# Optimization experiments

Measured on AMD Instinct MI355X. Metric: run time of the kernel, lower is better.

## Reference

```python
import jax, jax.numpy as jnp
import numpy as np

D_MODEL = 512
D_STATE = 128
D_CONV = 4
EXPAND = 2
HEADDIM = 64
NGROUPS = 1
D_INNER = EXPAND * D_MODEL            # 1024
NHEADS = D_INNER // HEADDIM           # 16
CONV_DIM = D_INNER + 2 * NGROUPS * D_STATE   # 1280
D_IN_PROJ = 2 * D_INNER + 2 * NGROUPS * D_STATE + NHEADS  # 2320
EPS = 1e-5


def _silu(v):
    return v * jax.nn.sigmoid(v)


def setup_inputs() -> dict:
    key = jax.random.key(0)
    ks = jax.random.split(key, 8)
    B, L = 2, 1024
    x = jax.random.normal(ks[0], (B, L, D_MODEL), jnp.float32)
    in_proj_w = jax.random.normal(ks[1], (D_IN_PROJ, D_MODEL), jnp.float32) * (D_MODEL ** -0.5)
    conv_w = jax.random.normal(ks[2], (CONV_DIM, D_CONV), jnp.float32) * (D_CONV ** -0.5)
    conv_b = jnp.zeros((CONV_DIM,), jnp.float32)
    # dt_bias = softplus^-1(dt) for dt ~ U[1e-3, 0.1]  (Mamba2 init)
    dt = jax.random.uniform(ks[3], (NHEADS,), jnp.float32, 0.001, 0.1)
    dt_bias = jnp.log(jnp.expm1(dt))
    A_log = jnp.log(jax.random.uniform(ks[4], (NHEADS,), jnp.float32, 1.0, 16.0))
    D = jnp.ones((NHEADS,), jnp.float32)
    norm_w = jnp.ones((D_INNER,), jnp.float32)
    out_proj_w = jax.random.normal(ks[5], (D_MODEL, D_INNER), jnp.float32) * (D_INNER ** -0.5)
    return dict(x=x, in_proj_w=in_proj_w, conv_w=conv_w, conv_b=conv_b,
                dt_bias=dt_bias, A_log=A_log, D=D, norm_w=norm_w, out_proj_w=out_proj_w)


def _mamba2(x, in_proj_w, conv_w, conv_b, dt_bias, A_log, D, norm_w, out_proj_w):
    Bb, L, _ = x.shape
    # input projection -> [z | xBC | dt]
    zxbcdt = jnp.einsum('bld,ed->ble', x, in_proj_w)          # (B,L,2320)
    z = zxbcdt[..., :D_INNER]                                  # (B,L,1024)
    xBC = zxbcdt[..., D_INNER:D_INNER + CONV_DIM]              # (B,L,1280)
    dt = jax.nn.softplus(zxbcdt[..., D_INNER + CONV_DIM:] + dt_bias)  # (B,L,H)
    # causal depthwise conv1d over L + SiLU
    lhs = jnp.transpose(xBC, (0, 2, 1))                        # (B,C,L)
    rhs = conv_w[:, None, :]                                   # (C,1,K)
    conv = jax.lax.conv_general_dilated(
        lhs, rhs, window_strides=(1,), padding=[(D_CONV - 1, 0)],
        dimension_numbers=('NCH', 'OIH', 'NCH'), feature_group_count=CONV_DIM)
    xBC = _silu(jnp.transpose(conv, (0, 2, 1)) + conv_b)       # (B,L,1280)
    xs = xBC[..., :D_INNER].reshape(Bb, L, NHEADS, HEADDIM)    # (B,L,H,P)
    Bmat = xBC[..., D_INNER:D_INNER + D_STATE]                 # (B,L,N) ngroups=1
    Cmat = xBC[..., D_INNER + D_STATE:]                        # (B,L,N)
    # selective scan: h_t = exp(dt_t*A)*h_{t-1} + (dt_t*x_t) outer B_t ; y_t = C_t . h_t
    A = -jnp.exp(A_log)                                        # (H,)
    dA = jnp.exp(dt * A)                                       # (B,L,H)
    dx = dt[..., None] * xs                                    # (B,L,H,P)

    def step(h, inp):
        dA_t, dx_t, B_t, C_t = inp                             # (B,H),(B,H,P),(B,N),(B,N)
        h = h * dA_t[..., None, None] + dx_t[..., None] * B_t[:, None, None, :]
        y = jnp.einsum('bhpn,bn->bhp', h, C_t)
        return h, y

    h0 = jnp.zeros((Bb, NHEADS, HEADDIM, D_STATE), x.dtype)
    _, ys = jax.lax.scan(step, h0, (jnp.moveaxis(dA, 1, 0), jnp.moveaxis(dx, 1, 0),
                                    jnp.moveaxis(Bmat, 1, 0), jnp.moveaxis(Cmat, 1, 0)))
    y = jnp.moveaxis(ys, 0, 1) + xs * D[None, None, :, None]   # (B,L,H,P)
    y = y.reshape(Bb, L, D_INNER)
    # gated RMSNorm: rmsnorm(y * silu(z)) * w
    g = y * _silu(z)
    g = g * jax.lax.rsqrt(jnp.mean(g * g, axis=-1, keepdims=True) + EPS) * norm_w
    return jnp.einsum('ble,de->bld', g, out_proj_w)            # (B,L,d_model)


def reference(x, in_proj_w, conv_w, conv_b, dt_bias, A_log, D, norm_w, out_proj_w):
    return _mamba2(x, in_proj_w, conv_w, conv_b, dt_bias, A_log, D, norm_w, out_proj_w)
```

## Files before the change

kernel.cpp:

```cpp
#include <hip/hip_runtime.h>
#include <math.h>

#define BATCH 2
#define SEQ 1024
#define DM 512
#define DI 1024
#define DS 128
#define NH 16
#define HD 64
#define CONVD 1280
#define DPROJ 2320
#define ROWS (BATCH*SEQ)
#define NCH 16
#define CHK 64
#define NPAD 2432

typedef unsigned short u16;
typedef unsigned int   u32;
typedef u16   u16x4 __attribute__((ext_vector_type(4)));
typedef u16   u16x8 __attribute__((ext_vector_type(8)));
typedef short bf16x8 __attribute__((ext_vector_type(8)));
typedef float f32x4 __attribute__((ext_vector_type(4)));

__device__ __forceinline__ u16 f2bf(float f) {
    u32 u = __float_as_uint(f);
    return (u16)((u + 0x7fffu + ((u >> 16) & 1u)) >> 16);
}
__device__ __forceinline__ float bf2f(u16 h) {
    return __uint_as_float(((u32)h) << 16);
}
__device__ __forceinline__ void gl_lds16(const u16* g, u16* lds) {
    __builtin_amdgcn_global_load_lds((const __attribute__((address_space(1))) void*)g,
                                     (__attribute__((address_space(3))) void*)lds,
                                     16, 0, 0);
}

__device__ __forceinline__ int xcd_swz(int bid, int nwg) {
    int q = nwg >> 3;
    return (bid & 7) * q + (bid >> 3);
}

__device__ __forceinline__ int swz_off(int row, int q, int SLROW) {
    return (row*SLROW + (q ^ (row & 7)))*8;
}
template<int SLROW>
__device__ __forceinline__ void stage64(const u16* gbase, int gstride, u16* lds, int tid) {
    #pragma unroll
    for (int j = 0; j < (64*SLROW)/256; ++j) {
        int slot = j*256 + tid;
        int row = slot / SLROW;
        int pos = slot % SLROW;
        gl_lds16(gbase + (size_t)row*gstride + (pos ^ (row & 7))*8, lds + slot*8);
    }
}

__device__ __forceinline__ void cvt_blk(const float* __restrict__ src,
                                        u16* __restrict__ dst,
                                        int blk, int n_src, int n_total) {
    int idx = (blk*256 + threadIdx.x)*8;
    if (idx >= n_total) return;
    u16x8 o;
    if (idx + 8 <= n_src) {
        float4 a = *reinterpret_cast<const float4*>(src + idx);
        float4 b = *reinterpret_cast<const float4*>(src + idx + 4);
        o[0]=f2bf(a.x); o[1]=f2bf(a.y); o[2]=f2bf(a.z); o[3]=f2bf(a.w);
        o[4]=f2bf(b.x); o[5]=f2bf(b.y); o[6]=f2bf(b.z); o[7]=f2bf(b.w);
    } else {
        #pragma unroll
        for (int e = 0; e < 8; ++e)
            o[e] = (idx + e < n_src) ? f2bf(src[idx + e]) : (u16)0;
    }
    *reinterpret_cast<u16x8*>(dst + idx) = o;
}

__global__ __launch_bounds__(256) void k_prep(const float* __restrict__ x,
                                              const float* __restrict__ W,
                                              const float* __restrict__ Wo,
                                              const float* __restrict__ dt_bias,
                                              const float* __restrict__ A_log,
                                              u16* __restrict__ xb,
                                              u16* __restrict__ Wb,
                                              u16* __restrict__ Wob,
                                              float* __restrict__ dtb,
                                              float* __restrict__ abuf) {
    int bid = blockIdx.x;
    if (bid < 512) { cvt_blk(x, xb, bid, ROWS*DM, ROWS*DM); return; }
    if (bid < 1120) { cvt_blk(W, Wb, bid-512, DPROJ*DM, NPAD*DM); return; }
    if (bid < 1376) { cvt_blk(Wo, Wob, bid-1120, DM*DI, DM*DI); return; }
    int wave = threadIdx.x >> 6, lane = threadIdx.x & 63;
    int row = (bid-1376)*4 + wave;
    int h = lane & 15, part = lane >> 4;
    const float* xr = x + (size_t)row * DM + part*128;
    const float* wr = W + (size_t)(DI + CONVD + h) * DM + part*128;
    float acc = 0.f;
    #pragma unroll 4
    for (int j = 0; j < 32; ++j) {
        float4 xv = *reinterpret_cast<const float4*>(xr + j*4);
        float4 wv = *reinterpret_cast<const float4*>(wr + j*4);
        acc += xv.x*wv.x + xv.y*wv.y + xv.z*wv.z + xv.w*wv.w;
    }
    acc += __shfl_xor(acc, 16);
    acc += __shfl_xor(acc, 32);
    if (part == 0) {
        float v = acc + dt_bias[h];
        float dt = (v > 20.f) ? v : log1pf(expf(v));
        dtb[row*NH + h]  = dt;
        abuf[row*NH + h] = dt * (-expf(A_log[h]));
    }
}

template<int BM, int BN, int K, int NBX, bool BF16OUT>
__global__ __launch_bounds__(256) void k_gemm(const u16* __restrict__ A,
                                              const u16* __restrict__ B,
                                              void* __restrict__ Cv,
                                              int ldc, int ncols) {
    constexpr int BK = 64;
    constexpr int NK = K / BK;
    constexpr int WTM = BM/2, WTN = BN/2, FM = WTM/16, FN = WTN/16;
    constexpr int CA = BM/32, CB = BN/32;
    constexpr int TA = BM*8, TB = BN*8;
    __shared__ u16 As[2*TA*8];
    __shared__ u16 Bs[2*TB*8];
    int tid = threadIdx.x, lane = tid & 63, wave = tid >> 6;
    int wr = wave >> 1, wc = wave & 1;

    int nb = xcd_swz(blockIdx.x, gridDim.x);
    size_t bm = (size_t)(nb / NBX) * BM, bn = (size_t)(nb % NBX) * BN;

    const u16* sA[CA]; int dA[CA];
    #pragma unroll
    for (int j = 0; j < CA; ++j) {
        int i = j*256 + tid, row = i >> 3, pos = i & 7;
        sA[j] = A + (bm + row)*(size_t)K + (pos ^ (row & 7))*8;
        dA[j] = i*8;
    }
    const u16* sB[CB]; int dB[CB];
    #pragma unroll
    for (int j = 0; j < CB; ++j) {
        int i = j*256 + tid, row = i >> 3, pos = i & 7;
        sB[j] = B + (bn + row)*(size_t)K + (pos ^ (row & 7))*8;
        dB[j] = i*8;
    }

    int fr = lane & 15, kq = lane >> 4;
    int ar[FM], br[FN];
    #pragma unroll
    for (int fi = 0; fi < FM; ++fi) ar[fi] = wr*WTM + fi*16 + fr;
    #pragma unroll
    for (int fj = 0; fj < FN; ++fj) br[fj] = wc*WTN + fj*16 + fr;

    f32x4 acc[FM][FN];
    #pragma unroll
    for (int fi = 0; fi < FM; ++fi)
        #pragma unroll
        for (int fj = 0; fj < FN; ++fj)
            acc[fi][fj] = (f32x4){0.f,0.f,0.f,0.f};

    #pragma unroll
    for (int j = 0; j < CA; ++j) gl_lds16(sA[j], As + dA[j]);
    #pragma unroll
    for (int j = 0; j < CB; ++j) gl_lds16(sB[j], Bs + dB[j]);
    asm volatile("s_waitcnt vmcnt(0)" ::: "memory");
    __builtin_amdgcn_s_barrier();

    int cur = 0;
    #pragma unroll 1
    for (int step = 0; step < NK; ++step) {
        if (step + 1 < NK) {
            int k0 = (step+1)*BK;
            int nbuf = cur ^ 1;
            #pragma unroll
            for (int j = 0; j < CA; ++j) gl_lds16(sA[j] + k0, As + nbuf*TA*8 + dA[j]);
            #pragma unroll
            for (int j = 0; j < CB; ++j) gl_lds16(sB[j] + k0, Bs + nbuf*TB*8 + dB[j]);
        }
        const u16* Ab = As + cur*TA*8;
        const u16* Bb = Bs + cur*TB*8;
        #pragma unroll
        for (int ks = 0; ks < 2; ++ks) {
            bf16x8 av[FM], bv[FN];
            #pragma unroll
            for (int fi = 0; fi < FM; ++fi)
                av[fi] = *reinterpret_cast<const bf16x8*>(Ab + (ar[fi]*8 + ((ks*4+kq) ^ (ar[fi]&7)))*8);
            #pragma unroll
            for (int fj = 0; fj < FN; ++fj)
                bv[fj] = *reinterpret_cast<const bf16x8*>(Bb + (br[fj]*8 + ((ks*4+kq) ^ (br[fj]&7)))*8);
            #pragma unroll
            for (int fi = 0; fi < FM; ++fi)
                #pragma unroll
                for (int fj = 0; fj < FN; ++fj)
                    acc[fi][fj] = __builtin_amdgcn_mfma_f32_16x16x32_bf16(
                        av[fi], bv[fj], acc[fi][fj], 0, 0, 0);
        }
        asm volatile("s_waitcnt vmcnt(0)" ::: "memory");
        __builtin_amdgcn_s_barrier();
        cur ^= 1;
    }

    #pragma unroll
    for (int fi = 0; fi < FM; ++fi) {
        size_t grow0 = bm + wr*WTM + fi*16 + kq*4;
        #pragma unroll
        for (int fj = 0; fj < FN; ++fj) {
            size_t gcol = bn + wc*WTN + fj*16 + fr;
            if ((int)gcol < ncols) {
                #pragma unroll
                for (int r = 0; r < 4; ++r) {
                    if constexpr (BF16OUT)
                        ((u16*)Cv)[(grow0 + r)*ldc + gcol] = f2bf(acc[fi][fj][r]);
                    else
                        ((float*)Cv)[(grow0 + r)*ldc + gcol] = acc[fi][fj][r];
                }
            }
        }
    }
}

__global__ __launch_bounds__(320) void k_conv(const u16* __restrict__ zx,
                                              const float* __restrict__ cw,
                                              const float* __restrict__ cb,
                                              u16* __restrict__ convo) {
    int row = blockIdx.x;
    int l   = row & (SEQ-1);
    int c0  = threadIdx.x * 4;

    const float4* cw4 = reinterpret_cast<const float4*>(cw);
    float4 w0 = cw4[c0+0], w1 = cw4[c0+1], w2 = cw4[c0+2], w3 = cw4[c0+3];
    const float* wa0 = &w0.x; const float* wa1 = &w1.x;
    const float* wa2 = &w2.x; const float* wa3 = &w3.x;

    float4 bv = *reinterpret_cast<const float4*>(cb + c0);
    float acc0 = bv.x, acc1 = bv.y, acc2 = bv.z, acc3 = bv.w;

    #pragma unroll
    for (int k = 0; k < 4; ++k) {
        int lk = l - 3 + k;
        if (lk < 0) continue;
        u16x4 v = *reinterpret_cast<const u16x4*>(zx + (size_t)(row-3+k)*DPROJ + DI + c0);
        acc0 += bf2f(v[0]) * wa0[k];
        acc1 += bf2f(v[1]) * wa1[k];
        acc2 += bf2f(v[2]) * wa2[k];
        acc3 += bf2f(v[3]) * wa3[k];
    }
    u16x4 o;
    o[0] = f2bf(acc0 / (1.f + expf(-acc0)));
    o[1] = f2bf(acc1 / (1.f + expf(-acc1)));
    o[2] = f2bf(acc2 / (1.f + expf(-acc2)));
    o[3] = f2bf(acc3 / (1.f + expf(-acc3)));
    *reinterpret_cast<u16x4*>(convo + (size_t)row*CONVD + c0) = o;
}

__global__ __launch_bounds__(256) void k_chunk_state(
    const u16* __restrict__ convo, const float* __restrict__ dtb,
    const float* __restrict__ abuf, u16* __restrict__ Sb,
    float* __restrict__ Pbuf) {
    int nb = xcd_swz(blockIdx.x, gridDim.x);
    int h  = nb & (NH-1);
    int c  = (nb >> 4) & (NCH-1);
    int b  = nb >> 8;
    int sidx = c + NCH*(h + NH*b);
    int row0 = b*SEQ + c*CHK;
    int tid = threadIdx.x, lane = tid & 63, wave = tid >> 6;
    int wr = wave >> 1, wc = wave & 1;

    __shared__ u16 xsT[64*64];
    __shared__ u16 BT[128*64];
    __shared__ float s_coef[CHK];

    int st = tid >> 2, q = tid & 3;
    const u16* r = convo + (size_t)(row0 + st)*CONVD;
    u16x8 xa = *reinterpret_cast<const u16x8*>(r + h*HD + q*16);
    u16x8 xc = *reinterpret_cast<const u16x8*>(r + h*HD + q*16 + 8);
    u16x8 b0 = *reinterpret_cast<const u16x8*>(r + DI + q*32);
    u16x8 b1 = *reinterpret_cast<const u16x8*>(r + DI + q*32 + 8);
    u16x8 b2 = *reinterpret_cast<const u16x8*>(r + DI + q*32 + 16);
    u16x8 b3 = *reinterpret_cast<const u16x8*>(r + DI + q*32 + 24);

    if (tid < CHK) {
        float v = abuf[(size_t)(row0 + tid)*NH + h];
        #pragma unroll
        for (int off = 1; off < 64; off <<= 1) {
            float o = __shfl_up(v, off);
            if (tid >= off) v += o;
        }
        float vend = __shfl(v, 63);
        float dt = dtb[(size_t)(row0 + tid)*NH + h];
        s_coef[tid] = dt * expf(vend - v);
        if (tid == 63) Pbuf[sidx] = expf(vend);
    }
    __syncthreads();

    float cf = s_coef[st];
    #pragma unroll
    for (int e = 0; e < 16; ++e) {
        int p = q*16 + e;
        u16 xv = (e < 8) ? xa[e] : xc[e-8];
        xsT[(p*8 + ((st>>3) ^ (p&7)))*8 + (st&7)] = f2bf(cf * bf2f(xv));
    }
    #pragma unroll
    for (int e = 0; e < 32; ++e) {
        int n = q*32 + e;
        u16 bvv = (e < 8) ? b0[e] : (e < 16) ? b1[e-8] : (e < 24) ? b2[e-16] : b3[e-24];
        BT[(n*8 + ((st>>3) ^ (n&7)))*8 + (st&7)] = bvv;
    }
    __syncthreads();

    int kq = lane >> 4, fr = lane & 15;
    f32x4 acc[2][4];
    #pragma unroll
    for (int fi = 0; fi < 2; ++fi)
        #pragma unroll
        for (int fj = 0; fj < 4; ++fj)
            acc[fi][fj] = (f32x4){0.f,0.f,0.f,0.f};

    #pragma unroll
    for (int ks = 0; ks < 2; ++ks) {
        bf16x8 av[2], bv[4];
        #pragma unroll
        for (int fi = 0; fi < 2; ++fi)
            av[fi] = *reinterpret_cast<const bf16x8*>(xsT + swz_off(wr*32 + fi*16 + fr, ks*4 + kq, 8));
        #pragma unroll
        for (int fj = 0; fj < 4; ++fj)
            bv[fj] = *reinterpret_cast<const bf16x8*>(BT + swz_off(wc*64 + fj*16 + fr, ks*4 + kq, 8));
        #pragma unroll
        for (int fi = 0; fi < 2; ++fi)
            #pragma unroll
            for (int fj = 0; fj < 4; ++fj)
                acc[fi][fj] = __builtin_amdgcn_mfma_f32_16x16x32_bf16(av[fi], bv[fj], acc[fi][fj], 0,0,0);
    }

    u16* outp = Sb + (size_t)sidx*(HD*DS);
    #pragma unroll
    for (int fi = 0; fi < 2; ++fi)
        #pragma unroll
        for (int rr = 0; rr < 4; ++rr) {
            int p = wr*32 + fi*16 + kq*4 + rr;
            #pragma unroll
            for (int fj = 0; fj < 4; ++fj) {
                int n = wc*64 + fj*16 + fr;
                outp[(size_t)p*DS + n] = f2bf(acc[fi][fj][rr]);
            }
        }
}

__global__ __launch_bounds__(256) void k_state_pass(u16* __restrict__ Sb,
                                                    const float* __restrict__ Pbuf) {
    int bh = blockIdx.x >> 3, seg = blockIdx.x & 7;
    int off = seg*1024 + threadIdx.x*4;
    u16x4 s[NCH];
    #pragma unroll
    for (int cc = 0; cc < NCH; ++cc)
        s[cc] = *reinterpret_cast<const u16x4*>(Sb + ((size_t)(bh*NCH + cc))*(HD*DS) + off);
    float hr[4] = {0.f,0.f,0.f,0.f};
    #pragma unroll
    for (int cc = 0; cc < NCH; ++cc) {
        u16x4 w = { f2bf(hr[0]), f2bf(hr[1]), f2bf(hr[2]), f2bf(hr[3]) };
        *reinterpret_cast<u16x4*>(Sb + ((size_t)(bh*NCH + cc))*(HD*DS) + off) = w;
        float P = Pbuf[bh*NCH + cc];
        #pragma unroll
        for (int j = 0; j < 4; ++j) hr[j] = hr[j]*P + bf2f(s[cc][j]);
    }
}

__global__ __launch_bounds__(256) void k_chunk_out(
    const u16* __restrict__ convo, const float* __restrict__ dtb,
    const float* __restrict__ abuf, const u16* __restrict__ Sb,
    const float* __restrict__ Dp, u16* __restrict__ ybuf) {
    int nb = xcd_swz(blockIdx.x, gridDim.x);
    int h  = nb & (NH-1);
    int c  = (nb >> 4) & (NCH-1);
    int b  = nb >> 8;
    int sidx = c + NCH*(h + NH*b);
    int row0 = b*SEQ + c*CHK;
    int tid = threadIdx.x, lane = tid & 63, wave = tid >> 6;
    int wr = wave >> 1, wc = wave & 1;

    __shared__ u16 Ct[64*128];
    __shared__ u16 Bh[64*128];
    __shared__ u16 Mt[64*64];
    __shared__ u16 dxT[64*64];
    __shared__ float s_cum[CHK];
    __shared__ float s_dt[CHK];

    const u16* cbase = convo + (size_t)row0*CONVD;

    stage64<16>(cbase + DI + DS, CONVD, Ct, tid);
    stage64<16>(cbase + DI,      CONVD, Bh, tid);

    int st = tid >> 2, q = tid & 3;
    u16x8 xr0 = *reinterpret_cast<const u16x8*>(cbase + (size_t)st*CONVD + h*HD + q*16);
    u16x8 xr1 = *reinterpret_cast<const u16x8*>(cbase + (size_t)st*CONVD + h*HD + q*16 + 8);

    if (tid < CHK) {
        float v = abuf[(size_t)(row0 + tid)*NH + h];
        #pragma unroll
        for (int off = 1; off < 64; off <<= 1) {
            float o = __shfl_up(v, off);
            if (tid >= off) v += o;
        }
        s_cum[tid] = v;
        s_dt[tid] = dtb[(size_t)(row0 + tid)*NH + h];
    }
    __syncthreads();

    #pragma unroll
    for (int e = 0; e < 16; ++e) {
        int p = q*16 + e;
        u16 xv = (e < 8) ? xr0[e] : xr1[e-8];
        dxT[(p*8 + ((st>>3) ^ (p&7)))*8 + (st&7)] = xv;
    }

    int kq = lane >> 4, fr = lane & 15;

    f32x4 macc[2][2];
    #pragma unroll
    for (int fi = 0; fi < 2; ++fi)
        #pragma unroll
        for (int fj = 0; fj < 2; ++fj)
            macc[fi][fj] = (f32x4){0.f,0.f,0.f,0.f};
    #pragma unroll
    for (int ks = 0; ks < 4; ++ks) {
        bf16x8 av[2], bv[2];
        #pragma unroll
        for (int fi = 0; fi < 2; ++fi)
            av[fi] = *reinterpret_cast<const bf16x8*>(Ct + swz_off(wr*32 + fi*16 + fr, ks*4 + kq, 16));
        #pragma unroll
        for (int fj = 0; fj < 2; ++fj)
            bv[fj] = *reinterpret_cast<const bf16x8*>(Bh + swz_off(wc*32 + fj*16 + fr, ks*4 + kq, 16));
        #pragma unroll
        for (int fi = 0; fi < 2; ++fi)
            #pragma unroll
            for (int fj = 0; fj < 2; ++fj)
                macc[fi][fj] = __builtin_amdgcn_mfma_f32_16x16x32_bf16(av[fi], bv[fj], macc[fi][fj], 0,0,0);
    }

    #pragma unroll
    for (int fi = 0; fi < 2; ++fi)
        #pragma unroll
        for (int rr = 0; rr < 4; ++rr) {
            int t = wr*32 + fi*16 + kq*4 + rr;
            float cumt = s_cum[t];
            #pragma unroll
            for (int fj = 0; fj < 2; ++fj) {
                int s = wc*32 + fj*16 + fr;
                float val = (s <= t) ? macc[fi][fj][rr] * expf(cumt - s_cum[s]) * s_dt[s] : 0.f;
                Mt[(t*8 + ((s>>3) ^ (t&7)))*8 + (s&7)] = f2bf(val);
            }
        }
    __syncthreads();

    stage64<16>(Sb + (size_t)sidx*(HD*DS), DS, Bh, tid);

    f32x4 accY[2][2];
    #pragma unroll
    for (int fi = 0; fi < 2; ++fi)
        #pragma unroll
        for (int fj = 0; fj < 2; ++fj)
            accY[fi][fj] = (f32x4){0.f,0.f,0.f,0.f};
    #pragma unroll
    for (int ks = 0; ks < 2; ++ks) {
        bf16x8 av[2], bv[2];
        #pragma unroll
        for (int fi = 0; fi < 2; ++fi)
            av[fi] = *reinterpret_cast<const bf16x8*>(Mt + swz_off(wr*32 + fi*16 + fr, ks*4 + kq, 8));
        #pragma unroll
        for (int fj = 0; fj < 2; ++fj)
            bv[fj] = *reinterpret_cast<const bf16x8*>(dxT + swz_off(wc*32 + fj*16 + fr, ks*4 + kq, 8));
        #pragma unroll
        for (int fi = 0; fi < 2; ++fi)
            #pragma unroll
            for (int fj = 0; fj < 2; ++fj)
                accY[fi][fj] = __builtin_amdgcn_mfma_f32_16x16x32_bf16(av[fi], bv[fj], accY[fi][fj], 0,0,0);
    }
    __syncthreads();

    f32x4 accD[2][2];
    #pragma unroll
    for (int fi = 0; fi < 2; ++fi)
        #pragma unroll
        for (int fj = 0; fj < 2; ++fj)
            accD[fi][fj] = (f32x4){0.f,0.f,0.f,0.f};
    #pragma unroll
    for (int ks = 0; ks < 4; ++ks) {
        bf16x8 av[2], bv[2];
        #pragma unroll
        for (int fi = 0; fi < 2; ++fi)
            av[fi] = *reinterpret_cast<const bf16x8*>(Ct + swz_off(wr*32 + fi*16 + fr, ks*4 + kq, 16));
        #pragma unroll
        for (int fj = 0; fj < 2; ++fj)
            bv[fj] = *reinterpret_cast<const bf16x8*>(Bh + swz_off(wc*32 + fj*16 + fr, ks*4 + kq, 16));
        #pragma unroll
        for (int fi = 0; fi < 2; ++fi)
            #pragma unroll
            for (int fj = 0; fj < 2; ++fj)
                accD[fi][fj] = __builtin_amdgcn_mfma_f32_16x16x32_bf16(av[fi], bv[fj], accD[fi][fj], 0,0,0);
    }

    float Dv = Dp[h];
    #pragma unroll
    for (int fi = 0; fi < 2; ++fi)
        #pragma unroll
        for (int rr = 0; rr < 4; ++rr) {
            int t = wr*32 + fi*16 + kq*4 + rr;
            float et = expf(s_cum[t]);
            #pragma unroll
            for (int fj = 0; fj < 2; ++fj) {
                int p = wc*32 + fj*16 + fr;
                float xs = bf2f(cbase[(size_t)t*CONVD + h*HD + p]);
                float y = accY[fi][fj][rr] + et*accD[fi][fj][rr] + Dv*xs;
                ybuf[(size_t)(row0 + t)*DI + h*HD + p] = f2bf(y);
            }
        }
}

__global__ __launch_bounds__(256) void k_gate(const u16* __restrict__ zx,
                                              const u16* __restrict__ ybuf,
                                              const float* __restrict__ nw,
                                              u16* __restrict__ g) {
    int row = blockIdx.x;
    int t = threadIdx.x;
    const u16* zr = zx + (size_t)row*DPROJ;
    const u16* yr = ybuf + (size_t)row*DI;

    u16x4 zv = *reinterpret_cast<const u16x4*>(zr + t*4);
    u16x4 yv = *reinterpret_cast<const u16x4*>(yr + t*4);
    float gv[4];
    float ss = 0.f;
    #pragma unroll
    for (int j = 0; j < 4; ++j) {
        float z = bf2f(zv[j]), y = bf2f(yv[j]);
        float sz = z / (1.f + expf(-z));
        float gg = y * sz;
        gv[j] = gg;
        ss += gg*gg;
    }
    ss += __shfl_xor(ss, 1);
    ss += __shfl_xor(ss, 2);
    ss += __shfl_xor(ss, 4);
    ss += __shfl_xor(ss, 8);
    ss += __shfl_xor(ss, 16);
    ss += __shfl_xor(ss, 32);
    __shared__ float ls[4];
    if ((t & 63) == 0) ls[t >> 6] = ss;
    __syncthreads();
    float tot = ls[0] + ls[1] + ls[2] + ls[3];
    float scale = rsqrtf(tot * (1.f/DI) + 1e-5f);

    float4 nv = *reinterpret_cast<const float4*>(nw + t*4);
    const float* na = &nv.x;
    u16x4 og = { f2bf(gv[0]*scale*na[0]), f2bf(gv[1]*scale*na[1]),
                 f2bf(gv[2]*scale*na[2]), f2bf(gv[3]*scale*na[3]) };
    *reinterpret_cast<u16x4*>(g + (size_t)row*DI + t*4) = og;
}

extern "C" void kernel_launch(void* const* d_in, const int* in_sizes, int n_in,
                              void* d_out, int out_size, void* d_ws, size_t ws_size,
                              hipStream_t stream) {
    const float* x         = (const float*)d_in[0];
    const float* in_proj_w = (const float*)d_in[1];
    const float* conv_w    = (const float*)d_in[2];
    const float* conv_b    = (const float*)d_in[3];
    const float* dt_bias   = (const float*)d_in[4];
    const float* A_log     = (const float*)d_in[5];
    const float* Dp        = (const float*)d_in[6];
    const float* norm_w    = (const float*)d_in[7];
    const float* out_proj_w= (const float*)d_in[8];
    float* out = (float*)d_out;

    char* p = (char*)d_ws;
    u16*   zxb   = (u16*)p;   p += (size_t)ROWS*DPROJ*2;
    u16*   convo = (u16*)p;   p += (size_t)ROWS*CONVD*2;
    float* dtb   = (float*)p; p += (size_t)ROWS*NH*4;
    float* abuf  = (float*)p; p += (size_t)ROWS*NH*4;
    u16*   ybuf  = (u16*)p;   p += (size_t)ROWS*DI*2;
    u16*   xb    = (u16*)p;   p += (size_t)ROWS*DM*2;
    u16*   Wb    = (u16*)p;   p += (size_t)NPAD*DM*2;
    u16*   Wob   = (u16*)p;   p += (size_t)DM*DI*2;
    u16*   Sb    = (u16*)p;   p += (size_t)BATCH*NH*NCH*HD*DS*2;
    float* Pbuf  = (float*)p; p += 512*4;
    u16*   gb    = (u16*)p;   p += (size_t)ROWS*DI*2;

    k_prep<<<1888, 256, 0, stream>>>(x, in_proj_w, out_proj_w, dt_bias, A_log,
                                     xb, Wb, Wob, dtb, abuf);

    k_gemm<64,128,512,19,true><<<(NPAD/128)*(ROWS/64), 256, 0, stream>>>(xb, Wb, zxb, DPROJ, DPROJ);

    k_conv<<<ROWS, CONVD/4, 0, stream>>>(zxb, conv_w, conv_b, convo);

    k_chunk_state<<<BATCH*NH*NCH, 256, 0, stream>>>(convo, dtb, abuf, Sb, Pbuf);
    k_state_pass <<<BATCH*NH*8, 256, 0, stream>>>(Sb, Pbuf);
    k_chunk_out  <<<BATCH*NH*NCH, 256, 0, stream>>>(convo, dtb, abuf, Sb, Dp, ybuf);

    k_gate<<<ROWS, 256, 0, stream>>>(zxb, ybuf, norm_w, gb);

    k_gemm<64,64,1024,8,false><<<(DM/64)*(ROWS/64), 256, 0, stream>>>(gb, Wob, out, DM, DM);
}
```

Baseline: 75.70 us.

## Fuse gated RMSNorm into out-projection GEMM, fold norm weight into Wo

Removes the separate gating/RMSNorm kernel. The out-projection GEMM now builds y*silu(z) on the fly while staging its A tile and accumulates per-row sums of squares during the K loop. The RMS scale is applied to the accumulator in the epilogue, and norm_w is folded into the bf16 weight conversion. This saves one launch and a full round trip of the gated tensor through global memory, but every N-block recomputes the silu gating (8x redundant) and the A staging is now register-based rather than direct-to-LDS.

```diff
diff --git a/kernel.cpp b/kernel.cpp
--- a/kernel.cpp
+++ b/kernel.cpp
@@ -76,6 +76,7 @@
 __global__ __launch_bounds__(256) void k_prep(const float* __restrict__ x,
                                               const float* __restrict__ W,
                                               const float* __restrict__ Wo,
+                                              const float* __restrict__ nw,
                                               const float* __restrict__ dt_bias,
                                               const float* __restrict__ A_log,
                                               u16* __restrict__ xb,
@@ -86,7 +87,19 @@
     int bid = blockIdx.x;
     if (bid < 512) { cvt_blk(x, xb, bid, ROWS*DM, ROWS*DM); return; }
     if (bid < 1120) { cvt_blk(W, Wb, bid-512, DPROJ*DM, NPAD*DM); return; }
-    if (bid < 1376) { cvt_blk(Wo, Wob, bid-1120, DM*DI, DM*DI); return; }
+    if (bid < 1376) {
+        int idx = ((bid-1120)*256 + threadIdx.x)*8;
+        int e = idx & (DI-1);
+        float4 a = *reinterpret_cast<const float4*>(Wo + idx);
+        float4 b = *reinterpret_cast<const float4*>(Wo + idx + 4);
+        float4 na = *reinterpret_cast<const float4*>(nw + e);
+        float4 nb = *reinterpret_cast<const float4*>(nw + e + 4);
+        u16x8 o;
+        o[0]=f2bf(a.x*na.x); o[1]=f2bf(a.y*na.y); o[2]=f2bf(a.z*na.z); o[3]=f2bf(a.w*na.w);
+        o[4]=f2bf(b.x*nb.x); o[5]=f2bf(b.y*nb.y); o[6]=f2bf(b.z*nb.z); o[7]=f2bf(b.w*nb.w);
+        *reinterpret_cast<u16x8*>(Wob + idx) = o;
+        return;
+    }
     int wave = threadIdx.x >> 6, lane = threadIdx.x & 63;
     int row = (bid-1376)*4 + wave;
     int h = lane & 15, part = lane >> 4;
@@ -216,6 +229,140 @@
     }
 }
 
+__global__ __launch_bounds__(256) void k_outproj_gate(
+    const u16* __restrict__ ybuf, const u16* __restrict__ zxb,
+    const u16* __restrict__ Wob, float* __restrict__ out) {
+    constexpr int BM=64, BN=64, K=1024, BK=64, NK=K/BK, NBX=DM/BN;
+    constexpr int FM=2, FN=2;
+    constexpr int TA = BM*8, TB = BN*8;
+    __shared__ u16 As[2*TA*8];
+    __shared__ u16 Bs[2*TB*8];
+    __shared__ float s_ssq[BM];
+    int tid = threadIdx.x, lane = tid & 63, wave = tid >> 6;
+    int wr = wave >> 1, wc = wave & 1;
+
+    int nb = xcd_swz(blockIdx.x, gridDim.x);
+    size_t bm = (size_t)(nb / NBX) * BM, bn = (size_t)(nb % NBX) * BN;
+
+    int r = tid >> 2, qd = tid & 3;
+    const u16* yrow = ybuf + (bm + r)*(size_t)DI + qd*16;
+    const u16* zrow = zxb + (bm + r)*(size_t)DPROJ + qd*16;
+    int aslot0 = (r*8 + ((2*qd)   ^ (r & 7)))*8;
+    int aslot1 = (r*8 + ((2*qd+1) ^ (r & 7)))*8;
+
+    const u16* sB[2]; int dB[2];
+    #pragma unroll
+    for (int j = 0; j < 2; ++j) {
+        int i = j*256 + tid, row = i >> 3, pos = i & 7;
+        sB[j] = Wob + (bn + row)*(size_t)K + (pos ^ (row & 7))*8;
+        dB[j] = i*8;
+    }
+
+    int fr = lane & 15, kq = lane >> 4;
+    int ar[FM], br[FN];
+    #pragma unroll
+    for (int fi = 0; fi < FM; ++fi) ar[fi] = wr*32 + fi*16 + fr;
+    #pragma unroll
+    for (int fj = 0; fj < FN; ++fj) br[fj] = wc*32 + fj*16 + fr;
+
+    f32x4 acc[FM][FN];
+    #pragma unroll
+    for (int fi = 0; fi < FM; ++fi)
+        #pragma unroll
+        for (int fj = 0; fj < FN; ++fj)
+            acc[fi][fj] = (f32x4){0.f,0.f,0.f,0.f};
+
+    float ssq = 0.f;
+    auto STAGE_A = [&](int buf, u16x8 ya, u16x8 yb, u16x8 za, u16x8 zb) {
+        u16x8 o0, o1;
+        #pragma unroll
+        for (int e = 0; e < 8; ++e) {
+            float y = bf2f(ya[e]), z = bf2f(za[e]);
+            float gg = y * (z / (1.f + expf(-z)));
+            ssq += gg*gg;
+            o0[e] = f2bf(gg);
+        }
+        #pragma unroll
+        for (int e = 0; e < 8; ++e) {
+            float y = bf2f(yb[e]), z = bf2f(zb[e]);
+            float gg = y * (z / (1.f + expf(-z)));
+            ssq += gg*gg;
+            o1[e] = f2bf(gg);
+        }
+        u16* dst = As + buf*TA*8;
+        *reinterpret_cast<u16x8*>(dst + aslot0) = o0;
+        *reinterpret_cast<u16x8*>(dst + aslot1) = o1;
+    };
+
+    #pragma unroll
+    for (int j = 0; j < 2; ++j) gl_lds16(sB[j], Bs + dB[j]);
+    {
+        u16x8 ya = *reinterpret_cast<const u16x8*>(yrow);
+        u16x8 yb = *reinterpret_cast<const u16x8*>(yrow + 8);
+        u16x8 za = *reinterpret_cast<const u16x8*>(zrow);
+        u16x8 zb = *reinterpret_cast<const u16x8*>(zrow + 8);
+        STAGE_A(0, ya, yb, za, zb);
+    }
+    __syncthreads();
+
+    int cur = 0;
+    #pragma unroll 1
+    for (int step = 0; step < NK; ++step) {
+        u16x8 nya, nyb, nza, nzb;
+        bool has_next = (step + 1 < NK);
+        if (has_next) {
+            int k0 = (step+1)*BK;
+            #pragma unroll
+            for (int j = 0; j < 2; ++j) gl_lds16(sB[j] + k0, Bs + (cur^1)*TB*8 + dB[j]);
+            nya = *reinterpret_cast<const u16x8*>(yrow + k0);
+            nyb = *reinterpret_cast<const u16x8*>(yrow + k0 + 8);
+            nza = *reinterpret_cast<const u16x8*>(zrow + k0);
+            nzb = *reinterpret_cast<const u16x8*>(zrow + k0 + 8);
+        }
+        const u16* Ab = As + cur*TA*8;
+        const u16* Bb = Bs + cur*TB*8;
+        #pragma unroll
+        for (int ks = 0; ks < 2; ++ks) {
+            bf16x8 av[FM], bv[FN];
+            #pragma unroll
+            for (int fi = 0; fi < FM; ++fi)
+                av[fi] = *reinterpret_cast<const bf16x8*>(Ab + (ar[fi]*8 + ((ks*4+kq) ^ (ar[fi]&7)))*8);
+            #pragma unroll
+            for (int fj = 0; fj < FN; ++fj)
+                bv[fj] = *reinterpret_cast<const bf16x8*>(Bb + (br[fj]*8 + ((ks*4+kq) ^ (br[fj]&7)))*8);
+            #pragma unroll
+            for (int fi = 0; fi < FM; ++fi)
+                #pragma unroll
+                for (int fj = 0; fj < FN; ++fj)
+                    acc[fi][fj] = __builtin_amdgcn_mfma_f32_16x16x32_bf16(
+                        av[fi], bv[fj], acc[fi][fj], 0, 0, 0);
+        }
+        if (has_next) STAGE_A(cur^1, nya, nyb, nza, nzb);
+        __syncthreads();
+        cur ^= 1;
+    }
+
+    ssq += __shfl_xor(ssq, 1);
+    ssq += __shfl_xor(ssq, 2);
+    if (qd == 0) s_ssq[r] = ssq;
+    __syncthreads();
+
+    #pragma unroll
+    for (int fi = 0; fi < FM; ++fi) {
+        #pragma unroll
+        for (int rr = 0; rr < 4; ++rr) {
+            int lr = wr*32 + fi*16 + kq*4 + rr;
+            float scale = rsqrtf(s_ssq[lr]*(1.f/DI) + 1e-5f);
+            size_t grow = bm + lr;
+            #pragma unroll
+            for (int fj = 0; fj < FN; ++fj) {
+                size_t gcol = bn + wc*32 + fj*16 + fr;
+                out[grow*DM + gcol] = scale * acc[fi][fj][rr];
+            }
+        }
+    }
+}
+
 __global__ __launch_bounds__(320) void k_conv(const u16* __restrict__ zx,
                                               const float* __restrict__ cw,
                                               const float* __restrict__ cb,
@@ -511,46 +658,6 @@
                 ybuf[(size_t)(row0 + t)*DI + h*HD + p] = f2bf(y);
             }
         }
-}
-
-__global__ __launch_bounds__(256) void k_gate(const u16* __restrict__ zx,
-                                              const u16* __restrict__ ybuf,
-                                              const float* __restrict__ nw,
-                                              u16* __restrict__ g) {
-    int row = blockIdx.x;
-    int t = threadIdx.x;
-    const u16* zr = zx + (size_t)row*DPROJ;
-    const u16* yr = ybuf + (size_t)row*DI;
-
-    u16x4 zv = *reinterpret_cast<const u16x4*>(zr + t*4);
-    u16x4 yv = *reinterpret_cast<const u16x4*>(yr + t*4);
-    float gv[4];
-    float ss = 0.f;
-    #pragma unroll
-    for (int j = 0; j < 4; ++j) {
-        float z = bf2f(zv[j]), y = bf2f(yv[j]);
-        float sz = z / (1.f + expf(-z));
-        float gg = y * sz;
-        gv[j] = gg;
-        ss += gg*gg;
-    }
-    ss += __shfl_xor(ss, 1);
-    ss += __shfl_xor(ss, 2);
-    ss += __shfl_xor(ss, 4);
-    ss += __shfl_xor(ss, 8);
-    ss += __shfl_xor(ss, 16);
-    ss += __shfl_xor(ss, 32);
-    __shared__ float ls[4];
-    if ((t & 63) == 0) ls[t >> 6] = ss;
-    __syncthreads();
-    float tot = ls[0] + ls[1] + ls[2] + ls[3];
-    float scale = rsqrtf(tot * (1.f/DI) + 1e-5f);
-
-    float4 nv = *reinterpret_cast<const float4*>(nw + t*4);
-    const float* na = &nv.x;
-    u16x4 og = { f2bf(gv[0]*scale*na[0]), f2bf(gv[1]*scale*na[1]),
-                 f2bf(gv[2]*scale*na[2]), f2bf(gv[3]*scale*na[3]) };
-    *reinterpret_cast<u16x4*>(g + (size_t)row*DI + t*4) = og;
 }
 
 extern "C" void kernel_launch(void* const* d_in, const int* in_sizes, int n_in,
@@ -578,9 +685,8 @@
     u16*   Wob   = (u16*)p;   p += (size_t)DM*DI*2;
     u16*   Sb    = (u16*)p;   p += (size_t)BATCH*NH*NCH*HD*DS*2;
     float* Pbuf  = (float*)p; p += 512*4;
-    u16*   gb    = (u16*)p;   p += (size_t)ROWS*DI*2;
-
-    k_prep<<<1888, 256, 0, stream>>>(x, in_proj_w, out_proj_w, dt_bias, A_log,
+
+    k_prep<<<1888, 256, 0, stream>>>(x, in_proj_w, out_proj_w, norm_w, dt_bias, A_log,
                                      xb, Wb, Wob, dtb, abuf);
 
     k_gemm<64,128,512,19,true><<<(NPAD/128)*(ROWS/64), 256, 0, stream>>>(xb, Wb, zxb, DPROJ, DPROJ);
@@ -591,7 +697,5 @@
     k_state_pass <<<BATCH*NH*8, 256, 0, stream>>>(Sb, Pbuf);
     k_chunk_out  <<<BATCH*NH*NCH, 256, 0, stream>>>(convo, dtb, abuf, Sb, Dp, ybuf);
 
-    k_gate<<<ROWS, 256, 0, stream>>>(zxb, ybuf, norm_w, gb);
-
-    k_gemm<64,64,1024,8,false><<<(DM/64)*(ROWS/64), 256, 0, stream>>>(gb, Wob, out, DM, DM);
-}
+    k_outproj_gate<<<(DM/64)*(ROWS/64), 256, 0, stream>>>(ybuf, zxb, Wob, out);
+}
```

Result: slower. 89.05 us (+17.6%).

## Fuse inter-chunk state scan into chunk output kernel, drop state-pass launch

Applied to the files above, without the earlier changes.

Removes the separate state-pass kernel, which did a sequential prefix scan over chunk states and wrote the carried states back. Each chunk-output block now computes its incoming state itself as a decay-weighted sum of all earlier chunk states, read directly from the per-chunk state buffer, and writes it into shared memory. This saves one kernel launch and a full read/write pass over the state buffer. In exchange the total state reads grow quadratically with chunk count, and later chunks do up to 15 serial loads, which makes the work uneven across blocks.

```diff
diff --git a/kernel.cpp b/kernel.cpp
--- a/kernel.cpp
+++ b/kernel.cpp
@@ -343,34 +343,15 @@
         }
 }
 
-__global__ __launch_bounds__(256) void k_state_pass(u16* __restrict__ Sb,
-                                                    const float* __restrict__ Pbuf) {
-    int bh = blockIdx.x >> 3, seg = blockIdx.x & 7;
-    int off = seg*1024 + threadIdx.x*4;
-    u16x4 s[NCH];
-    #pragma unroll
-    for (int cc = 0; cc < NCH; ++cc)
-        s[cc] = *reinterpret_cast<const u16x4*>(Sb + ((size_t)(bh*NCH + cc))*(HD*DS) + off);
-    float hr[4] = {0.f,0.f,0.f,0.f};
-    #pragma unroll
-    for (int cc = 0; cc < NCH; ++cc) {
-        u16x4 w = { f2bf(hr[0]), f2bf(hr[1]), f2bf(hr[2]), f2bf(hr[3]) };
-        *reinterpret_cast<u16x4*>(Sb + ((size_t)(bh*NCH + cc))*(HD*DS) + off) = w;
-        float P = Pbuf[bh*NCH + cc];
-        #pragma unroll
-        for (int j = 0; j < 4; ++j) hr[j] = hr[j]*P + bf2f(s[cc][j]);
-    }
-}
-
 __global__ __launch_bounds__(256) void k_chunk_out(
     const u16* __restrict__ convo, const float* __restrict__ dtb,
     const float* __restrict__ abuf, const u16* __restrict__ Sb,
+    const float* __restrict__ Pbuf,
     const float* __restrict__ Dp, u16* __restrict__ ybuf) {
     int nb = xcd_swz(blockIdx.x, gridDim.x);
     int h  = nb & (NH-1);
     int c  = (nb >> 4) & (NCH-1);
     int b  = nb >> 8;
-    int sidx = c + NCH*(h + NH*b);
     int row0 = b*SEQ + c*CHK;
     int tid = threadIdx.x, lane = tid & 63, wave = tid >> 6;
     int wr = wave >> 1, wc = wave & 1;
@@ -449,7 +430,43 @@
         }
     __syncthreads();
 
-    stage64<16>(Sb + (size_t)sidx*(HD*DS), DS, Bh, tid);
+    {
+        int off0[4];
+        #pragma unroll
+        for (int j = 0; j < 4; ++j) {
+            int slot = j*256 + tid;
+            int row = slot >> 4, pos = slot & 15;
+            off0[j] = row*DS + ((pos ^ (row & 7))*8);
+        }
+        float accf[4][8];
+        #pragma unroll
+        for (int j = 0; j < 4; ++j)
+            #pragma unroll
+            for (int e = 0; e < 8; ++e) accf[j][e] = 0.f;
+
+        const float* Pb = Pbuf + NCH*(h + NH*b);
+        const u16* Sbase = Sb + (size_t)(NCH*(h + NH*b))*(HD*DS);
+        float w = 1.f;
+        #pragma unroll 1
+        for (int cc = c-1; cc >= 0; --cc) {
+            const u16* sc = Sbase + (size_t)cc*(HD*DS);
+            #pragma unroll
+            for (int j = 0; j < 4; ++j) {
+                u16x8 v = *reinterpret_cast<const u16x8*>(sc + off0[j]);
+                #pragma unroll
+                for (int e = 0; e < 8; ++e) accf[j][e] += w * bf2f(v[e]);
+            }
+            w *= Pb[cc];
+        }
+        #pragma unroll
+        for (int j = 0; j < 4; ++j) {
+            int slot = j*256 + tid;
+            u16x8 o;
+            #pragma unroll
+            for (int e = 0; e < 8; ++e) o[e] = f2bf(accf[j][e]);
+            *reinterpret_cast<u16x8*>(Bh + slot*8) = o;
+        }
+    }
 
     f32x4 accY[2][2];
     #pragma unroll
@@ -588,8 +605,7 @@
     k_conv<<<ROWS, CONVD/4, 0, stream>>>(zxb, conv_w, conv_b, convo);
 
     k_chunk_state<<<BATCH*NH*NCH, 256, 0, stream>>>(convo, dtb, abuf, Sb, Pbuf);
-    k_state_pass <<<BATCH*NH*8, 256, 0, stream>>>(Sb, Pbuf);
-    k_chunk_out  <<<BATCH*NH*NCH, 256, 0, stream>>>(convo, dtb, abuf, Sb, Dp, ybuf);
+    k_chunk_out  <<<BATCH*NH*NCH, 256, 0, stream>>>(convo, dtb, abuf, Sb, Pbuf, Dp, ybuf);
 
     k_gate<<<ROWS, 256, 0, stream>>>(zxb, ybuf, norm_w, gb);
 
```

New measurement: 78.17 us. +3.3%, slower.

## Triple-buffer GEMM LDS staging with partial vmcnt waits

Applied to the files above, without the earlier changes.

Changes the k_gemm main loop from double buffering to three LDS stages, issuing loads two steps ahead and waiting only until the current stage's loads have landed (vmcnt counts) rather than draining all outstanding loads. This lets global-to-LDS copies overlap more with MFMA work. It costs 1.5x the LDS per block, which may reduce occupancy, and relies on the vmcnt templates covering every CA+CB combination used.

```diff
diff --git a/kernel.cpp b/kernel.cpp
--- a/kernel.cpp
+++ b/kernel.cpp
@@ -33,6 +33,14 @@
     __builtin_amdgcn_global_load_lds((const __attribute__((address_space(1))) void*)g,
                                      (__attribute__((address_space(3))) void*)lds,
                                      16, 0, 0);
+}
+
+template<int N> __device__ __forceinline__ void wait_vmcnt() {
+    if constexpr (N == 0)  asm volatile("s_waitcnt vmcnt(0)"  ::: "memory");
+    else if constexpr (N == 4)  asm volatile("s_waitcnt vmcnt(4)"  ::: "memory");
+    else if constexpr (N == 6)  asm volatile("s_waitcnt vmcnt(6)"  ::: "memory");
+    else if constexpr (N == 8)  asm volatile("s_waitcnt vmcnt(8)"  ::: "memory");
+    else if constexpr (N == 12) asm volatile("s_waitcnt vmcnt(12)" ::: "memory");
 }
 
 __device__ __forceinline__ int xcd_swz(int bid, int nwg) {
@@ -119,8 +127,8 @@
     constexpr int WTM = BM/2, WTN = BN/2, FM = WTM/16, FN = WTN/16;
     constexpr int CA = BM/32, CB = BN/32;
     constexpr int TA = BM*8, TB = BN*8;
-    __shared__ u16 As[2*TA*8];
-    __shared__ u16 Bs[2*TB*8];
+    __shared__ u16 As[3*TA*8];
+    __shared__ u16 Bs[3*TB*8];
     int tid = threadIdx.x, lane = tid & 63, wave = tid >> 6;
     int wr = wave >> 1, wc = wave & 1;
 
@@ -156,26 +164,28 @@
         for (int fj = 0; fj < FN; ++fj)
             acc[fi][fj] = (f32x4){0.f,0.f,0.f,0.f};
 
-    #pragma unroll
-    for (int j = 0; j < CA; ++j) gl_lds16(sA[j], As + dA[j]);
-    #pragma unroll
-    for (int j = 0; j < CB; ++j) gl_lds16(sB[j], Bs + dB[j]);
-    asm volatile("s_waitcnt vmcnt(0)" ::: "memory");
-    __builtin_amdgcn_s_barrier();
-
-    int cur = 0;
+    auto STAGE = [&](int t, int buf) {
+        int k0 = t*BK;
+        #pragma unroll
+        for (int j = 0; j < CA; ++j) gl_lds16(sA[j] + k0, As + buf*TA*8 + dA[j]);
+        #pragma unroll
+        for (int j = 0; j < CB; ++j) gl_lds16(sB[j] + k0, Bs + buf*TB*8 + dB[j]);
+    };
+
+    STAGE(0, 0);
+    if (NK > 1) STAGE(1, 1);
+
     #pragma unroll 1
     for (int step = 0; step < NK; ++step) {
-        if (step + 1 < NK) {
-            int k0 = (step+1)*BK;
-            int nbuf = cur ^ 1;
-            #pragma unroll
-            for (int j = 0; j < CA; ++j) gl_lds16(sA[j] + k0, As + nbuf*TA*8 + dA[j]);
-            #pragma unroll
-            for (int j = 0; j < CB; ++j) gl_lds16(sB[j] + k0, Bs + nbuf*TB*8 + dB[j]);
-        }
-        const u16* Ab = As + cur*TA*8;
-        const u16* Bb = Bs + cur*TB*8;
+        int nxt = step + 2;
+        if (nxt < NK) STAGE(nxt, nxt % 3);
+        if (step < NK-2)       wait_vmcnt<2*(CA+CB)>();
+        else if (step == NK-2) wait_vmcnt<CA+CB>();
+        else                   wait_vmcnt<0>();
+        __builtin_amdgcn_s_barrier();
+
+        const u16* Ab = As + (step % 3)*TA*8;
+        const u16* Bb = Bs + (step % 3)*TB*8;
         #pragma unroll
         for (int ks = 0; ks < 2; ++ks) {
             bf16x8 av[FM], bv[FN];
@@ -192,9 +202,7 @@
                     acc[fi][fj] = __builtin_amdgcn_mfma_f32_16x16x32_bf16(
                         av[fi], bv[fj], acc[fi][fj], 0, 0, 0);
         }
-        asm volatile("s_waitcnt vmcnt(0)" ::: "memory");
         __builtin_amdgcn_s_barrier();
-        cur ^= 1;
     }
 
     #pragma unroll
```

Result: slower. 79.31 us (+4.8%).
